# Kernel tuning notes

Measured on AMD Instinct MI355X. Metric: run time of the kernel, lower is better.

Reference implementation:

```python
import jax, jax.numpy as jnp
import numpy as np

B, N = 4, 8192


def setup_inputs() -> dict:
    key = jax.random.key(0)
    k1, k2, k3 = jax.random.split(key, 3)
    pc_pred = jax.random.normal(k1, (B, N, 3), dtype=jnp.float32)
    pc_target = jax.random.normal(k2, (B, N, 3), dtype=jnp.float32)
    fbpp = jax.random.uniform(k3, (B,), dtype=jnp.float32)
    return {"pc_pred": pc_pred, "pc_target": pc_target, "fbpp": fbpp, "lam": 1}


def _chamfer(x, y):
    # x: (B, N, 3), y: (B, M, 3)
    x2 = jnp.sum(x * x, axis=-1)                     # (B, N)
    y2 = jnp.sum(y * y, axis=-1)                     # (B, M)
    xy = jnp.einsum('bnd,bmd->bnm', x, y)            # (B, N, M)
    d2 = jnp.maximum(x2[:, :, None] + y2[:, None, :] - 2.0 * xy, 0.0)
    cham_x = jnp.mean(jnp.min(d2, axis=2), axis=1)   # (B,) pred -> target
    cham_y = jnp.mean(jnp.min(d2, axis=1), axis=1)   # (B,) target -> pred
    return jnp.mean(cham_x + cham_y)                 # scalar (batch mean)


def reference(pc_pred, pc_target, fbpp, lam):
    d = _chamfer(pc_pred, pc_target)
    r = jnp.mean(fbpp)
    return d + lam * r
```

## Files before the change

kernel.cpp:

```cpp
#include <hip/hip_runtime.h>
#include <math.h>


typedef __attribute__((ext_vector_type(8)))  short  short8;
typedef __attribute__((ext_vector_type(16))) float  f32x16;

#define YS      4
#define RPB     256

#define MFMA2(da, db, A, B0, B1) \
    asm("v_mfma_f32_32x32x16_bf16 %0, %2, %3, 0\n\t" \
        "v_mfma_f32_32x32x16_bf16 %1, %2, %4, 0\n\t" \
        "s_nop 7\n\t" \
        "s_nop 7" \
        : "=&v"(da), "=&v"(db) \
        : "v"(A), "v"(B0), "v"(B1))

static __device__ __forceinline__ float min3f(float a, float b, float c) {
    float d;
    asm("v_min3_f32 %0, %1, %2, %3" : "=v"(d) : "v"(a), "v"(b), "v"(c));
    return d;
}

static inline int roundup_h(int v, int a) { return (v + a - 1) / a * a; }

static __device__ __forceinline__ unsigned short f2bf(float f) {
    union { float f; unsigned int u; } v; v.f = f;
    unsigned int r = v.u + 0x7FFFu + ((v.u >> 16) & 1u);
    return (unsigned short)(r >> 16);
}
static __device__ __forceinline__ float bf2f(unsigned short s) {
    union { unsigned int u; float f; } v; v.u = ((unsigned int)s) << 16;
    return v.f;
}
static __device__ __forceinline__ unsigned int pk2(unsigned short lo,
                                                   unsigned short hi) {
    return (unsigned int)lo | ((unsigned int)hi << 16);
}

static __device__ __forceinline__ float allmin32(float v) {
    union { float f; int i; } u, t;
    u.f = v;
    t.i = __builtin_amdgcn_update_dpp(u.i, u.i, 0xB1, 0xF, 0xF, false);
    u.f = fminf(u.f, t.f);
    t.i = __builtin_amdgcn_update_dpp(u.i, u.i, 0x4E, 0xF, 0xF, false);
    u.f = fminf(u.f, t.f);
    t.i = __builtin_amdgcn_update_dpp(u.i, u.i, 0x124, 0xF, 0xF, false);
    u.f = fminf(u.f, t.f);
    t.i = __builtin_amdgcn_update_dpp(u.i, u.i, 0x128, 0xF, 0xF, false);
    u.f = fminf(u.f, t.f);
    t.i = __builtin_amdgcn_ds_swizzle(u.i, 0x401F);
    u.f = fminf(u.f, t.f);
    return u.f;
}

__global__ __launch_bounds__(256) void pack_kernel(
    const float* __restrict__ pred, const float* __restrict__ targ,
    int B, int N, int M, int NpadP, int NpadT,
    unsigned short* __restrict__ aP, unsigned short* __restrict__ bP,
    unsigned short* __restrict__ aT, unsigned short* __restrict__ bT)
{
    const int padmax = (NpadP > NpadT) ? NpadP : NpadT;
    const int gid = blockIdx.x * 256 + threadIdx.x;
    if (gid >= B * padmax) return;
    const int b = gid / padmax, i = gid - b * padmax;

    for (int cloud = 0; cloud < 2; ++cloud) {
        const int cnt  = cloud ? M : N;
        const int npad = cloud ? NpadT : NpadP;
        if (i >= npad) continue;
        const float* src = (cloud ? targ : pred) +
                           ((size_t)b * cnt + min(i, cnt - 1)) * 3;
        unsigned short* A  = (cloud ? aT : aP) + ((size_t)b * npad + i) * 16;
        unsigned short* Bk = (cloud ? bT : bP) + (size_t)b * npad * 16;

        const float xs[3] = {src[0], src[1], src[2]};
        const float n2 = xs[0]*xs[0] + xs[1]*xs[1] + xs[2]*xs[2];
        unsigned short th[3], tl[3], yh[3], yl[3];
        #pragma unroll
        for (int c = 0; c < 3; ++c) {
            const float t = -2.0f * xs[c];
            th[c] = f2bf(t);     tl[c] = f2bf(t - bf2f(th[c]));
            yh[c] = f2bf(xs[c]); yl[c] = f2bf(xs[c] - bf2f(yh[c]));
        }
        const unsigned short n2h = f2bf(n2);
        const unsigned short n2l = f2bf(n2 - bf2f(n2h));
        const unsigned short ONE = 0x3F80;

        uint4 alo, ahi, blo, bhi;
        alo.x = pk2(th[0], th[1]); alo.y = pk2(th[2], tl[0]);
        alo.z = pk2(tl[1], tl[2]); alo.w = pk2(th[0], th[1]);
        ahi.x = pk2(th[2], tl[0]); ahi.y = pk2(tl[1], tl[2]);
        ahi.z = pk2(ONE,  ONE);    ahi.w = pk2(n2h,  n2l);
        blo.x = pk2(yh[0], yh[1]); blo.y = pk2(yh[2], yh[0]);
        blo.z = pk2(yh[1], yh[2]); blo.w = pk2(yl[0], yl[1]);
        bhi.x = pk2(yl[2], yl[0]); bhi.y = pk2(yl[1], yl[2]);
        bhi.z = pk2(n2h,  n2l);    bhi.w = pk2(ONE,  ONE);

        *(uint4*)(A)     = alo;  *(uint4*)(A + 8) = ahi;
        const size_t tb = (size_t)(i >> 5) * 64 + (i & 31);
        *(uint4*)(Bk + tb * 8)        = blo;
        *(uint4*)(Bk + (tb + 32) * 8) = bhi;
    }
}

__global__ __launch_bounds__(256, 4) void mfma_sweep(
    const unsigned short* __restrict__ aP, const unsigned short* __restrict__ bP,
    const unsigned short* __restrict__ aT, const unsigned short* __restrict__ bT,
    int B, int N, int M, int NpadP, int NpadT, int NpadMax,
    float* __restrict__ rowpart)
{
    const int tid  = threadIdx.x;
    const int w    = tid >> 6;
    const int lane = tid & 63;
    const int lc   = lane & 31, h = lane >> 5;

    const int SP = NpadMax / RPB;
    int t = blockIdx.x;
    const int sp  = t % SP;  t /= SP;
    const int js  = t % YS;  t /= YS;
    const int b   = t % B;   t /= B;
    const int dir = t;

    const unsigned short* Xp = (dir == 0) ? aP : aT;
    const unsigned short* Yp = (dir == 0) ? bT : bP;
    const int NpadX = (dir == 0) ? NpadP : NpadT;
    const int NpadY = (dir == 0) ? NpadT : NpadP;
    const int Nx    = (dir == 0) ? N : M;
    if (sp * RPB >= NpadX) return;

    const int TM  = NpadY / 32;
    const int nt0 = TM / YS;
    const int t0  = js * nt0;

    const int row0 = sp * RPB + w * 64;
    const size_t abase = ((size_t)b * NpadX + row0 + lc) * 16 + (size_t)h * 8;
    const short8 a0 = *reinterpret_cast<const short8*>(Xp + abase);
    const short8 a1 = *reinterpret_cast<const short8*>(Xp + abase + 32 * 16);

    f32x16 rm0, rm1;
    #pragma unroll
    for (int r = 0; r < 16; ++r) {
        rm0[r] = __builtin_inff(); rm1[r] = __builtin_inff();
    }

    const unsigned short* yp =
        Yp + (size_t)b * NpadY * 16 + (size_t)t0 * 512 + (size_t)lane * 8;
    short8 c0 = *reinterpret_cast<const short8*>(yp);
    short8 c1 = *reinterpret_cast<const short8*>(yp + 512);

    for (int j = 0; j < nt0; j += 2) {
        const short8 n0 = *reinterpret_cast<const short8*>(yp + 1024);
        const short8 n1 = *reinterpret_cast<const short8*>(yp + 1536);
        yp += 1024;
        __builtin_amdgcn_sched_barrier(0);
        {
            f32x16 da, db;
            MFMA2(da, db, a0, c0, c1);
            #pragma unroll
            for (int r = 0; r < 16; ++r)
                rm0[r] = min3f(da[r], db[r], rm0[r]);
        }
        {
            f32x16 da, db;
            MFMA2(da, db, a1, c0, c1);
            #pragma unroll
            for (int r = 0; r < 16; ++r)
                rm1[r] = min3f(da[r], db[r], rm1[r]);
        }
        c0 = n0; c1 = n1;
    }

    const size_t outb = (((size_t)dir * B + b) * YS + js) * (size_t)NpadMax;
    #pragma unroll
    for (int r = 0; r < 16; ++r) {
        const float v0 = allmin32(rm0[r]);
        const float v1 = allmin32(rm1[r]);
        if (lc == 0) {
            const int rr = (r & 3) + 8 * (r >> 2) + 4 * h;
            const int ra = row0 + rr, rb = row0 + 32 + rr;
            if (ra < Nx) rowpart[outb + ra] = v0;
            if (rb < Nx) rowpart[outb + rb] = v1;
        }
    }
}

__global__ __launch_bounds__(256) void combine_kernel(
    const float* __restrict__ rowpart, int B, int N, int M,
    int NpadP, int NpadT, int NpadMax,
    float invBN, float invBM, float* __restrict__ partial)
{
    const int tid = threadIdx.x;
    const int tot = 2 * B * NpadMax;
    float acc = 0.f;
    for (int idx = blockIdx.x * 256 + tid; idx < tot; idx += gridDim.x * 256) {
        const int row = idx % NpadMax;
        const int rem = idx / NpadMax;
        const int b   = rem % B;
        const int dir = rem / B;
        const int Nx  = (dir == 0) ? N : M;
        if (row >= Nx) continue;
        float m = __builtin_inff();
        #pragma unroll
        for (int js = 0; js < YS; ++js)
            m = fminf(m, rowpart[(((size_t)dir * B + b) * YS + js)
                                 * (size_t)NpadMax + row]);
        acc += fmaxf(m, 0.f) * ((dir == 0) ? invBN : invBM);
    }
    __shared__ float sb[256];
    sb[tid] = acc; __syncthreads();
    for (int off2 = 128; off2 > 0; off2 >>= 1) {
        if (tid < off2) sb[tid] += sb[tid + off2];
        __syncthreads();
    }
    if (tid == 0) partial[blockIdx.x] = sb[0];
}

__global__ void finalize_kernel(const float* __restrict__ partial, int np,
                                const float* __restrict__ fbpp, int Bf,
                                const void* __restrict__ lamp,
                                float* __restrict__ out)
{
    __shared__ float sb[256];
    const int tid = threadIdx.x;
    float acc = 0.f;
    for (int i = tid; i < np; i += 256) acc += partial[i];
    sb[tid] = acc;
    __syncthreads();
    for (int off = 128; off > 0; off >>= 1) {
        if (tid < off) sb[tid] += sb[tid + off];
        __syncthreads();
    }
    if (tid == 0) {
        const int li = *(const int*)lamp;
        const float lam = (li >= -1000000 && li <= 1000000)
                            ? (float)li : *(const float*)lamp;
        float fm = 0.f;
        for (int i = 0; i < Bf; ++i) fm += fbpp[i];
        fm /= (float)Bf;
        out[0] = sb[0] + lam * fm;
    }
}

extern "C" void kernel_launch(void* const* d_in, const int* in_sizes, int n_in,
                              void* d_out, int out_size, void* d_ws, size_t ws_size,
                              hipStream_t stream) {
    const float* pred = (const float*)d_in[0];
    const float* targ = (const float*)d_in[1];
    const float* fbpp = (const float*)d_in[2];
    const void*  lamp = d_in[3];

    const int B = in_sizes[2];
    const int N = in_sizes[0] / (3 * B);
    const int M = in_sizes[1] / (3 * B);
    const int NpadP = roundup_h(N, RPB);
    const int NpadT = roundup_h(M, RPB);
    const int NpadMax = (NpadP > NpadT) ? NpadP : NpadT;

    size_t o = 0;
    auto take = [&](size_t bytes) {
        size_t r = o; o += (bytes + 255) & ~(size_t)255; return r;
    };
    unsigned short* aP = (unsigned short*)((char*)d_ws +
                         take((size_t)B * NpadP * 32 + 8192));
    unsigned short* bP = (unsigned short*)((char*)d_ws +
                         take((size_t)B * NpadP * 32 + 8192));
    unsigned short* aT = (unsigned short*)((char*)d_ws +
                         take((size_t)B * NpadT * 32 + 8192));
    unsigned short* bT = (unsigned short*)((char*)d_ws +
                         take((size_t)B * NpadT * 32 + 8192));
    float* rowpart = (float*)((char*)d_ws +
                     take((size_t)2 * B * YS * NpadMax * sizeof(float)));
    float* partial = (float*)((char*)d_ws + take(256 * sizeof(float)));
    (void)ws_size;

    pack_kernel<<<(B * NpadMax + 255) / 256, 256, 0, stream>>>(
        pred, targ, B, N, M, NpadP, NpadT, aP, bP, aT, bT);

    const int SP = NpadMax / RPB;
    const int blocks = 2 * B * YS * SP;
    mfma_sweep<<<blocks, 256, 0, stream>>>(
        aP, bP, aT, bT, B, N, M, NpadP, NpadT, NpadMax, rowpart);

    combine_kernel<<<256, 256, 0, stream>>>(
        rowpart, B, N, M, NpadP, NpadT, NpadMax,
        1.f / ((float)B * (float)N), 1.f / ((float)B * (float)M), partial);

    finalize_kernel<<<1, 256, 0, stream>>>(partial, 256, fbpp, B, lamp,
                                           (float*)d_out);
}
```

Before: 38.52 us.

## Fuse point packing into the MFMA sweep, staging Y tiles in LDS

Drops the separate pack kernel and its global workspace. Each sweep block now builds its bf16 split A fragments in registers and packs Y tiles into shared memory in chunks of 32 tiles, with block-wide syncs around each chunk. The Y split is doubled to 8 to raise the block count, which shortens each block's loop and doubles the rowpart traffic. This saves one launch and a global round trip, but every block repacks the same Y points and adds LDS reads and barriers inside the hot loop.

Measured after the change: 39.09 us. About the same (+1.5%).

```diff
diff --git a/kernel.cpp b/kernel.cpp
--- a/kernel.cpp
+++ b/kernel.cpp
@@ -5,8 +5,9 @@
 typedef __attribute__((ext_vector_type(8)))  short  short8;
 typedef __attribute__((ext_vector_type(16))) float  f32x16;
 
-#define YS      4
+#define YS      8
 #define RPB     256
+#define LTILES  32
 
 #define MFMA2(da, db, A, B0, B1) \
     asm("v_mfma_f32_32x32x16_bf16 %0, %2, %3, 0\n\t" \
@@ -54,59 +55,25 @@
     return u.f;
 }
 
-__global__ __launch_bounds__(256) void pack_kernel(
+struct PiecesT {
+    unsigned short th[3], tl[3], yh[3], yl[3], n2h, n2l;
+};
+static __device__ __forceinline__ PiecesT pieces(float x, float y, float z) {
+    PiecesT p;
+    const float xs[3] = {x, y, z};
+    const float n2 = x*x + y*y + z*z;
+    #pragma unroll
+    for (int c = 0; c < 3; ++c) {
+        const float t = -2.0f * xs[c];
+        p.th[c] = f2bf(t);      p.tl[c] = f2bf(t - bf2f(p.th[c]));
+        p.yh[c] = f2bf(xs[c]);  p.yl[c] = f2bf(xs[c] - bf2f(p.yh[c]));
+    }
+    p.n2h = f2bf(n2); p.n2l = f2bf(n2 - bf2f(p.n2h));
+    return p;
+}
+
+__global__ __launch_bounds__(256, 4) void fused_sweep(
     const float* __restrict__ pred, const float* __restrict__ targ,
-    int B, int N, int M, int NpadP, int NpadT,
-    unsigned short* __restrict__ aP, unsigned short* __restrict__ bP,
-    unsigned short* __restrict__ aT, unsigned short* __restrict__ bT)
-{
-    const int padmax = (NpadP > NpadT) ? NpadP : NpadT;
-    const int gid = blockIdx.x * 256 + threadIdx.x;
-    if (gid >= B * padmax) return;
-    const int b = gid / padmax, i = gid - b * padmax;
-
-    for (int cloud = 0; cloud < 2; ++cloud) {
-        const int cnt  = cloud ? M : N;
-        const int npad = cloud ? NpadT : NpadP;
-        if (i >= npad) continue;
-        const float* src = (cloud ? targ : pred) +
-                           ((size_t)b * cnt + min(i, cnt - 1)) * 3;
-        unsigned short* A  = (cloud ? aT : aP) + ((size_t)b * npad + i) * 16;
-        unsigned short* Bk = (cloud ? bT : bP) + (size_t)b * npad * 16;
-
-        const float xs[3] = {src[0], src[1], src[2]};
-        const float n2 = xs[0]*xs[0] + xs[1]*xs[1] + xs[2]*xs[2];
-        unsigned short th[3], tl[3], yh[3], yl[3];
-        #pragma unroll
-        for (int c = 0; c < 3; ++c) {
-            const float t = -2.0f * xs[c];
-            th[c] = f2bf(t);     tl[c] = f2bf(t - bf2f(th[c]));
-            yh[c] = f2bf(xs[c]); yl[c] = f2bf(xs[c] - bf2f(yh[c]));
-        }
-        const unsigned short n2h = f2bf(n2);
-        const unsigned short n2l = f2bf(n2 - bf2f(n2h));
-        const unsigned short ONE = 0x3F80;
-
-        uint4 alo, ahi, blo, bhi;
-        alo.x = pk2(th[0], th[1]); alo.y = pk2(th[2], tl[0]);
-        alo.z = pk2(tl[1], tl[2]); alo.w = pk2(th[0], th[1]);
-        ahi.x = pk2(th[2], tl[0]); ahi.y = pk2(tl[1], tl[2]);
-        ahi.z = pk2(ONE,  ONE);    ahi.w = pk2(n2h,  n2l);
-        blo.x = pk2(yh[0], yh[1]); blo.y = pk2(yh[2], yh[0]);
-        blo.z = pk2(yh[1], yh[2]); blo.w = pk2(yl[0], yl[1]);
-        bhi.x = pk2(yl[2], yl[0]); bhi.y = pk2(yl[1], yl[2]);
-        bhi.z = pk2(n2h,  n2l);    bhi.w = pk2(ONE,  ONE);
-
-        *(uint4*)(A)     = alo;  *(uint4*)(A + 8) = ahi;
-        const size_t tb = (size_t)(i >> 5) * 64 + (i & 31);
-        *(uint4*)(Bk + tb * 8)        = blo;
-        *(uint4*)(Bk + (tb + 32) * 8) = bhi;
-    }
-}
-
-__global__ __launch_bounds__(256, 4) void mfma_sweep(
-    const unsigned short* __restrict__ aP, const unsigned short* __restrict__ bP,
-    const unsigned short* __restrict__ aT, const unsigned short* __restrict__ bT,
     int B, int N, int M, int NpadP, int NpadT, int NpadMax,
     float* __restrict__ rowpart)
 {
@@ -122,21 +89,38 @@
     const int b   = t % B;   t /= B;
     const int dir = t;
 
-    const unsigned short* Xp = (dir == 0) ? aP : aT;
-    const unsigned short* Yp = (dir == 0) ? bT : bP;
+    const float* __restrict__ xsrc = (dir == 0) ? pred : targ;
+    const float* __restrict__ ysrc = (dir == 0) ? targ : pred;
+    const int Nx  = (dir == 0) ? N : M;
+    const int My  = (dir == 0) ? M : N;
     const int NpadX = (dir == 0) ? NpadP : NpadT;
     const int NpadY = (dir == 0) ? NpadT : NpadP;
-    const int Nx    = (dir == 0) ? N : M;
     if (sp * RPB >= NpadX) return;
 
     const int TM  = NpadY / 32;
     const int nt0 = TM / YS;
     const int t0  = js * nt0;
 
+    __shared__ unsigned short ypack[LTILES * 32 * 16];
+
+    const unsigned short ONE = 0x3F80;
     const int row0 = sp * RPB + w * 64;
-    const size_t abase = ((size_t)b * NpadX + row0 + lc) * 16 + (size_t)h * 8;
-    const short8 a0 = *reinterpret_cast<const short8*>(Xp + abase);
-    const short8 a1 = *reinterpret_cast<const short8*>(Xp + abase + 32 * 16);
+    short8 a0, a1;
+    #pragma unroll
+    for (int s = 0; s < 2; ++s) {
+        const int row = min(row0 + s * 32 + lc, Nx - 1);
+        const float* sx = xsrc + ((size_t)b * Nx + row) * 3;
+        const PiecesT p = pieces(sx[0], sx[1], sx[2]);
+        short8 v;
+        if (h == 0) {
+            v[0]=p.th[0]; v[1]=p.th[1]; v[2]=p.th[2]; v[3]=p.tl[0];
+            v[4]=p.tl[1]; v[5]=p.tl[2]; v[6]=p.th[0]; v[7]=p.th[1];
+        } else {
+            v[0]=p.th[2]; v[1]=p.tl[0]; v[2]=p.tl[1]; v[3]=p.tl[2];
+            v[4]=ONE;     v[5]=ONE;     v[6]=p.n2h;   v[7]=p.n2l;
+        }
+        if (s == 0) a0 = v; else a1 = v;
+    }
 
     f32x16 rm0, rm1;
     #pragma unroll
@@ -144,31 +128,47 @@
         rm0[r] = __builtin_inff(); rm1[r] = __builtin_inff();
     }
 
-    const unsigned short* yp =
-        Yp + (size_t)b * NpadY * 16 + (size_t)t0 * 512 + (size_t)lane * 8;
-    short8 c0 = *reinterpret_cast<const short8*>(yp);
-    short8 c1 = *reinterpret_cast<const short8*>(yp + 512);
-
-    for (int j = 0; j < nt0; j += 2) {
-        const short8 n0 = *reinterpret_cast<const short8*>(yp + 1024);
-        const short8 n1 = *reinterpret_cast<const short8*>(yp + 1536);
-        yp += 1024;
-        __builtin_amdgcn_sched_barrier(0);
-        {
-            f32x16 da, db;
-            MFMA2(da, db, a0, c0, c1);
-            #pragma unroll
-            for (int r = 0; r < 16; ++r)
-                rm0[r] = min3f(da[r], db[r], rm0[r]);
-        }
-        {
-            f32x16 da, db;
-            MFMA2(da, db, a1, c0, c1);
-            #pragma unroll
-            for (int r = 0; r < 16; ++r)
-                rm1[r] = min3f(da[r], db[r], rm1[r]);
-        }
-        c0 = n0; c1 = n1;
+    for (int f0 = 0; f0 < nt0; f0 += LTILES) {
+        const int fc = min(LTILES, nt0 - f0);
+        __syncthreads();
+        for (int i = tid; i < fc * 32; i += 256) {
+            const int gi  = min((t0 + f0) * 32 + i, My - 1);
+            const float* sy = ysrc + ((size_t)b * My + gi) * 3;
+            const PiecesT p = pieces(sy[0], sy[1], sy[2]);
+            uint4 blo, bhi;
+            blo.x = pk2(p.yh[0], p.yh[1]); blo.y = pk2(p.yh[2], p.yh[0]);
+            blo.z = pk2(p.yh[1], p.yh[2]); blo.w = pk2(p.yl[0], p.yl[1]);
+            bhi.x = pk2(p.yl[2], p.yl[0]); bhi.y = pk2(p.yl[1], p.yl[2]);
+            bhi.z = pk2(p.n2h,  p.n2l);    bhi.w = pk2(ONE,  ONE);
+            const int tile = i >> 5, pos = i & 31;
+            uint4* base = (uint4*)&ypack[(size_t)tile * 512];
+            base[pos]      = blo;
+            base[32 + pos] = bhi;
+        }
+        __syncthreads();
+
+        const unsigned short* lp = ypack + (size_t)lane * 8;
+        #pragma unroll 4
+        for (int j = 0; j < fc; j += 2) {
+            const short8 c0 = *reinterpret_cast<const short8*>(lp + (size_t)j * 512);
+            const short8 c1 = (j + 1 < fc)
+                ? *reinterpret_cast<const short8*>(lp + (size_t)(j + 1) * 512)
+                : c0;
+            {
+                f32x16 da, db;
+                MFMA2(da, db, a0, c0, c1);
+                #pragma unroll
+                for (int r = 0; r < 16; ++r)
+                    rm0[r] = min3f(da[r], db[r], rm0[r]);
+            }
+            {
+                f32x16 da, db;
+                MFMA2(da, db, a1, c0, c1);
+                #pragma unroll
+                for (int r = 0; r < 16; ++r)
+                    rm1[r] = min3f(da[r], db[r], rm1[r]);
+            }
+        }
     }
 
     const size_t outb = (((size_t)dir * B + b) * YS + js) * (size_t)NpadMax;
@@ -187,8 +187,7 @@
 
 __global__ __launch_bounds__(256) void combine_kernel(
     const float* __restrict__ rowpart, int B, int N, int M,
-    int NpadP, int NpadT, int NpadMax,
-    float invBN, float invBM, float* __restrict__ partial)
+    int NpadMax, float invBN, float invBM, float* __restrict__ partial)
 {
     const int tid = threadIdx.x;
     const int tot = 2 * B * NpadMax;
@@ -257,33 +256,17 @@
     const int NpadT = roundup_h(M, RPB);
     const int NpadMax = (NpadP > NpadT) ? NpadP : NpadT;
 
-    size_t o = 0;
-    auto take = [&](size_t bytes) {
-        size_t r = o; o += (bytes + 255) & ~(size_t)255; return r;
-    };
-    unsigned short* aP = (unsigned short*)((char*)d_ws +
-                         take((size_t)B * NpadP * 32 + 8192));
-    unsigned short* bP = (unsigned short*)((char*)d_ws +
-                         take((size_t)B * NpadP * 32 + 8192));
-    unsigned short* aT = (unsigned short*)((char*)d_ws +
-                         take((size_t)B * NpadT * 32 + 8192));
-    unsigned short* bT = (unsigned short*)((char*)d_ws +
-                         take((size_t)B * NpadT * 32 + 8192));
-    float* rowpart = (float*)((char*)d_ws +
-                     take((size_t)2 * B * YS * NpadMax * sizeof(float)));
-    float* partial = (float*)((char*)d_ws + take(256 * sizeof(float)));
+    float* rowpart = (float*)d_ws;
+    float* partial = rowpart + (size_t)2 * B * YS * NpadMax;
     (void)ws_size;
-
-    pack_kernel<<<(B * NpadMax + 255) / 256, 256, 0, stream>>>(
-        pred, targ, B, N, M, NpadP, NpadT, aP, bP, aT, bT);
 
     const int SP = NpadMax / RPB;
     const int blocks = 2 * B * YS * SP;
-    mfma_sweep<<<blocks, 256, 0, stream>>>(
-        aP, bP, aT, bT, B, N, M, NpadP, NpadT, NpadMax, rowpart);
+    fused_sweep<<<blocks, 256, 0, stream>>>(
+        pred, targ, B, N, M, NpadP, NpadT, NpadMax, rowpart);
 
     combine_kernel<<<256, 256, 0, stream>>>(
-        rowpart, B, N, M, NpadP, NpadT, NpadMax,
+        rowpart, B, N, M, NpadMax,
         1.f / ((float)B * (float)N), 1.f / ((float)B * (float)M), partial);
 
     finalize_kernel<<<1, 256, 0, stream>>>(partial, 256, fbpp, B, lamp,
```

## Compute both chamfer directions from one distance sweep via column minima

Applied to the files above, without the earlier changes.

Drops the second (target→pred) MFMA sweep. The single pred×target sweep now also reduces each tile's columns in registers, stages them in a shared-memory buffer, and writes per-row-block column minima to a new colpart array that combine_kernel reduces over SP. This roughly halves the MFMA work and the packing work. In exchange it adds about 32 min3 ops per iteration, a shared buffer that may lower occupancy, and extra colpart memory traffic. The number of column splits YS also goes from 4 to 8 to keep enough blocks in the grid.

Result: slower. 42.78 us (+11.1%).

```diff
diff --git a/kernel.cpp b/kernel.cpp
--- a/kernel.cpp
+++ b/kernel.cpp
@@ -5,7 +5,7 @@
 typedef __attribute__((ext_vector_type(8)))  short  short8;
 typedef __attribute__((ext_vector_type(16))) float  f32x16;
 
-#define YS      4
+#define YS      8
 #define RPB     256
 
 #define MFMA2(da, db, A, B0, B1) \
@@ -57,47 +57,53 @@
 __global__ __launch_bounds__(256) void pack_kernel(
     const float* __restrict__ pred, const float* __restrict__ targ,
     int B, int N, int M, int NpadP, int NpadT,
-    unsigned short* __restrict__ aP, unsigned short* __restrict__ bP,
-    unsigned short* __restrict__ aT, unsigned short* __restrict__ bT)
+    unsigned short* __restrict__ aP, unsigned short* __restrict__ bT)
 {
     const int padmax = (NpadP > NpadT) ? NpadP : NpadT;
     const int gid = blockIdx.x * 256 + threadIdx.x;
     if (gid >= B * padmax) return;
     const int b = gid / padmax, i = gid - b * padmax;
 
-    for (int cloud = 0; cloud < 2; ++cloud) {
-        const int cnt  = cloud ? M : N;
-        const int npad = cloud ? NpadT : NpadP;
-        if (i >= npad) continue;
-        const float* src = (cloud ? targ : pred) +
-                           ((size_t)b * cnt + min(i, cnt - 1)) * 3;
-        unsigned short* A  = (cloud ? aT : aP) + ((size_t)b * npad + i) * 16;
-        unsigned short* Bk = (cloud ? bT : bP) + (size_t)b * npad * 16;
-
+    const unsigned short ONE = 0x3F80;
+
+    if (i < NpadP) {
+        const float* src = pred + ((size_t)b * N + min(i, N - 1)) * 3;
+        unsigned short* A = aP + ((size_t)b * NpadP + i) * 16;
         const float xs[3] = {src[0], src[1], src[2]};
         const float n2 = xs[0]*xs[0] + xs[1]*xs[1] + xs[2]*xs[2];
-        unsigned short th[3], tl[3], yh[3], yl[3];
+        unsigned short th[3], tl[3];
         #pragma unroll
         for (int c = 0; c < 3; ++c) {
             const float t = -2.0f * xs[c];
-            th[c] = f2bf(t);     tl[c] = f2bf(t - bf2f(th[c]));
-            yh[c] = f2bf(xs[c]); yl[c] = f2bf(xs[c] - bf2f(yh[c]));
+            th[c] = f2bf(t); tl[c] = f2bf(t - bf2f(th[c]));
         }
         const unsigned short n2h = f2bf(n2);
         const unsigned short n2l = f2bf(n2 - bf2f(n2h));
-        const unsigned short ONE = 0x3F80;
-
-        uint4 alo, ahi, blo, bhi;
+        uint4 alo, ahi;
         alo.x = pk2(th[0], th[1]); alo.y = pk2(th[2], tl[0]);
         alo.z = pk2(tl[1], tl[2]); alo.w = pk2(th[0], th[1]);
         ahi.x = pk2(th[2], tl[0]); ahi.y = pk2(tl[1], tl[2]);
         ahi.z = pk2(ONE,  ONE);    ahi.w = pk2(n2h,  n2l);
+        *(uint4*)(A) = alo;  *(uint4*)(A + 8) = ahi;
+    }
+
+    if (i < NpadT) {
+        const float* src = targ + ((size_t)b * M + min(i, M - 1)) * 3;
+        unsigned short* Bk = bT + (size_t)b * NpadT * 16;
+        const float xs[3] = {src[0], src[1], src[2]};
+        const float n2 = xs[0]*xs[0] + xs[1]*xs[1] + xs[2]*xs[2];
+        unsigned short yh[3], yl[3];
+        #pragma unroll
+        for (int c = 0; c < 3; ++c) {
+            yh[c] = f2bf(xs[c]); yl[c] = f2bf(xs[c] - bf2f(yh[c]));
+        }
+        const unsigned short n2h = f2bf(n2);
+        const unsigned short n2l = f2bf(n2 - bf2f(n2h));
+        uint4 blo, bhi;
         blo.x = pk2(yh[0], yh[1]); blo.y = pk2(yh[2], yh[0]);
         blo.z = pk2(yh[1], yh[2]); blo.w = pk2(yl[0], yl[1]);
         bhi.x = pk2(yl[2], yl[0]); bhi.y = pk2(yl[1], yl[2]);
         bhi.z = pk2(n2h,  n2l);    bhi.w = pk2(ONE,  ONE);
-
-        *(uint4*)(A)     = alo;  *(uint4*)(A + 8) = ahi;
         const size_t tb = (size_t)(i >> 5) * 64 + (i & 31);
         *(uint4*)(Bk + tb * 8)        = blo;
         *(uint4*)(Bk + (tb + 32) * 8) = bhi;
@@ -105,38 +111,32 @@
 }
 
 __global__ __launch_bounds__(256, 4) void mfma_sweep(
-    const unsigned short* __restrict__ aP, const unsigned short* __restrict__ bP,
-    const unsigned short* __restrict__ aT, const unsigned short* __restrict__ bT,
-    int B, int N, int M, int NpadP, int NpadT, int NpadMax,
-    float* __restrict__ rowpart)
+    const unsigned short* __restrict__ aP, const unsigned short* __restrict__ bT,
+    int B, int N, int M, int NpadP, int NpadT, int NpadMax, int SP,
+    float* __restrict__ rowpart, float* __restrict__ colpart)
 {
     const int tid  = threadIdx.x;
     const int w    = tid >> 6;
     const int lane = tid & 63;
     const int lc   = lane & 31, h = lane >> 5;
 
-    const int SP = NpadMax / RPB;
     int t = blockIdx.x;
     const int sp  = t % SP;  t /= SP;
     const int js  = t % YS;  t /= YS;
-    const int b   = t % B;   t /= B;
-    const int dir = t;
-
-    const unsigned short* Xp = (dir == 0) ? aP : aT;
-    const unsigned short* Yp = (dir == 0) ? bT : bP;
-    const int NpadX = (dir == 0) ? NpadP : NpadT;
-    const int NpadY = (dir == 0) ? NpadT : NpadP;
-    const int Nx    = (dir == 0) ? N : M;
-    if (sp * RPB >= NpadX) return;
-
-    const int TM  = NpadY / 32;
+    const int b   = t;
+
+    if (sp * RPB >= NpadP) return;
+
+    const int TM  = NpadT / 32;
     const int nt0 = TM / YS;
     const int t0  = js * nt0;
 
+    __shared__ float colbuf[8][1024];
+
     const int row0 = sp * RPB + w * 64;
-    const size_t abase = ((size_t)b * NpadX + row0 + lc) * 16 + (size_t)h * 8;
-    const short8 a0 = *reinterpret_cast<const short8*>(Xp + abase);
-    const short8 a1 = *reinterpret_cast<const short8*>(Xp + abase + 32 * 16);
+    const size_t abase = ((size_t)b * NpadP + row0 + lc) * 16 + (size_t)h * 8;
+    const short8 a0 = *reinterpret_cast<const short8*>(aP + abase);
+    const short8 a1 = *reinterpret_cast<const short8*>(aP + abase + 32 * 16);
 
     f32x16 rm0, rm1;
     #pragma unroll
@@ -145,7 +145,7 @@
     }
 
     const unsigned short* yp =
-        Yp + (size_t)b * NpadY * 16 + (size_t)t0 * 512 + (size_t)lane * 8;
+        bT + (size_t)b * NpadT * 16 + (size_t)t0 * 512 + (size_t)lane * 8;
     short8 c0 = *reinterpret_cast<const short8*>(yp);
     short8 c1 = *reinterpret_cast<const short8*>(yp + 512);
 
@@ -154,12 +154,29 @@
         const short8 n1 = *reinterpret_cast<const short8*>(yp + 1536);
         yp += 1024;
         __builtin_amdgcn_sched_barrier(0);
+        float cmA, cmB;
         {
             f32x16 da, db;
             MFMA2(da, db, a0, c0, c1);
             #pragma unroll
             for (int r = 0; r < 16; ++r)
                 rm0[r] = min3f(da[r], db[r], rm0[r]);
+            cmA = min3f(da[0], da[1], da[2]);
+            cmA = min3f(cmA, da[3],  da[4]);
+            cmA = min3f(cmA, da[5],  da[6]);
+            cmA = min3f(cmA, da[7],  da[8]);
+            cmA = min3f(cmA, da[9],  da[10]);
+            cmA = min3f(cmA, da[11], da[12]);
+            cmA = min3f(cmA, da[13], da[14]);
+            cmA = min3f(cmA, da[15], cmA);
+            cmB = min3f(db[0], db[1], db[2]);
+            cmB = min3f(cmB, db[3],  db[4]);
+            cmB = min3f(cmB, db[5],  db[6]);
+            cmB = min3f(cmB, db[7],  db[8]);
+            cmB = min3f(cmB, db[9],  db[10]);
+            cmB = min3f(cmB, db[11], db[12]);
+            cmB = min3f(cmB, db[13], db[14]);
+            cmB = min3f(cmB, db[15], cmB);
         }
         {
             f32x16 da, db;
@@ -167,11 +184,29 @@
             #pragma unroll
             for (int r = 0; r < 16; ++r)
                 rm1[r] = min3f(da[r], db[r], rm1[r]);
-        }
+            cmA = min3f(cmA, da[0],  da[1]);
+            cmA = min3f(cmA, da[2],  da[3]);
+            cmA = min3f(cmA, da[4],  da[5]);
+            cmA = min3f(cmA, da[6],  da[7]);
+            cmA = min3f(cmA, da[8],  da[9]);
+            cmA = min3f(cmA, da[10], da[11]);
+            cmA = min3f(cmA, da[12], da[13]);
+            cmA = min3f(cmA, da[14], da[15]);
+            cmB = min3f(cmB, db[0],  db[1]);
+            cmB = min3f(cmB, db[2],  db[3]);
+            cmB = min3f(cmB, db[4],  db[5]);
+            cmB = min3f(cmB, db[6],  db[7]);
+            cmB = min3f(cmB, db[8],  db[9]);
+            cmB = min3f(cmB, db[10], db[11]);
+            cmB = min3f(cmB, db[12], db[13]);
+            cmB = min3f(cmB, db[14], db[15]);
+        }
+        colbuf[w * 2 + h][j * 32 + lc] = cmA;
+        if (j + 1 < nt0) colbuf[w * 2 + h][(j + 1) * 32 + lc] = cmB;
         c0 = n0; c1 = n1;
     }
 
-    const size_t outb = (((size_t)dir * B + b) * YS + js) * (size_t)NpadMax;
+    const size_t outb = ((size_t)b * YS + js) * (size_t)NpadMax;
     #pragma unroll
     for (int r = 0; r < 16; ++r) {
         const float v0 = allmin32(rm0[r]);
@@ -179,33 +214,51 @@
         if (lc == 0) {
             const int rr = (r & 3) + 8 * (r >> 2) + 4 * h;
             const int ra = row0 + rr, rb = row0 + 32 + rr;
-            if (ra < Nx) rowpart[outb + ra] = v0;
-            if (rb < Nx) rowpart[outb + rb] = v1;
-        }
+            if (ra < N) rowpart[outb + ra] = v0;
+            if (rb < N) rowpart[outb + rb] = v1;
+        }
+    }
+
+    __syncthreads();
+    const int nc = nt0 * 32;
+    const size_t coutb = ((size_t)b * SP + sp) * (size_t)NpadMax;
+    for (int c = tid; c < nc; c += 256) {
+        float m = colbuf[0][c];
+        #pragma unroll
+        for (int s = 1; s < 8; ++s) m = fminf(m, colbuf[s][c]);
+        const int gcol = t0 * 32 + c;
+        if (gcol < M) colpart[coutb + gcol] = m;
     }
 }
 
 __global__ __launch_bounds__(256) void combine_kernel(
-    const float* __restrict__ rowpart, int B, int N, int M,
-    int NpadP, int NpadT, int NpadMax,
+    const float* __restrict__ rowpart, const float* __restrict__ colpart,
+    int B, int N, int M, int NpadMax, int SP,
     float invBN, float invBM, float* __restrict__ partial)
 {
     const int tid = threadIdx.x;
-    const int tot = 2 * B * NpadMax;
+    const int per = B * NpadMax;
+    const int tot = 2 * per;
     float acc = 0.f;
     for (int idx = blockIdx.x * 256 + tid; idx < tot; idx += gridDim.x * 256) {
-        const int row = idx % NpadMax;
-        const int rem = idx / NpadMax;
-        const int b   = rem % B;
-        const int dir = rem / B;
-        const int Nx  = (dir == 0) ? N : M;
-        if (row >= Nx) continue;
-        float m = __builtin_inff();
-        #pragma unroll
-        for (int js = 0; js < YS; ++js)
-            m = fminf(m, rowpart[(((size_t)dir * B + b) * YS + js)
-                                 * (size_t)NpadMax + row]);
-        acc += fmaxf(m, 0.f) * ((dir == 0) ? invBN : invBM);
+        const int half = idx / per;
+        const int rem  = idx - half * per;
+        const int b    = rem / NpadMax;
+        const int p    = rem - b * NpadMax;
+        if (half == 0) {
+            if (p >= N) continue;
+            float m = __builtin_inff();
+            #pragma unroll
+            for (int js = 0; js < YS; ++js)
+                m = fminf(m, rowpart[((size_t)b * YS + js) * NpadMax + p]);
+            acc += fmaxf(m, 0.f) * invBN;
+        } else {
+            if (p >= M) continue;
+            float m = __builtin_inff();
+            for (int s = 0; s < SP; ++s)
+                m = fminf(m, colpart[((size_t)b * SP + s) * NpadMax + p]);
+            acc += fmaxf(m, 0.f) * invBM;
+        }
     }
     __shared__ float sb[256];
     sb[tid] = acc; __syncthreads();
@@ -256,6 +309,7 @@
     const int NpadP = roundup_h(N, RPB);
     const int NpadT = roundup_h(M, RPB);
     const int NpadMax = (NpadP > NpadT) ? NpadP : NpadT;
+    const int SP = NpadP / RPB;
 
     size_t o = 0;
     auto take = [&](size_t bytes) {
@@ -263,27 +317,24 @@
     };
     unsigned short* aP = (unsigned short*)((char*)d_ws +
                          take((size_t)B * NpadP * 32 + 8192));
-    unsigned short* bP = (unsigned short*)((char*)d_ws +
-                         take((size_t)B * NpadP * 32 + 8192));
-    unsigned short* aT = (unsigned short*)((char*)d_ws +
-                         take((size_t)B * NpadT * 32 + 8192));
     unsigned short* bT = (unsigned short*)((char*)d_ws +
                          take((size_t)B * NpadT * 32 + 8192));
     float* rowpart = (float*)((char*)d_ws +
-                     take((size_t)2 * B * YS * NpadMax * sizeof(float)));
+                     take((size_t)B * YS * NpadMax * sizeof(float)));
+    float* colpart = (float*)((char*)d_ws +
+                     take((size_t)B * SP * NpadMax * sizeof(float)));
     float* partial = (float*)((char*)d_ws + take(256 * sizeof(float)));
     (void)ws_size;
 
     pack_kernel<<<(B * NpadMax + 255) / 256, 256, 0, stream>>>(
-        pred, targ, B, N, M, NpadP, NpadT, aP, bP, aT, bT);
-
-    const int SP = NpadMax / RPB;
-    const int blocks = 2 * B * YS * SP;
+        pred, targ, B, N, M, NpadP, NpadT, aP, bT);
+
+    const int blocks = B * YS * SP;
     mfma_sweep<<<blocks, 256, 0, stream>>>(
-        aP, bP, aT, bT, B, N, M, NpadP, NpadT, NpadMax, rowpart);
+        aP, bT, B, N, M, NpadP, NpadT, NpadMax, SP, rowpart, colpart);
 
     combine_kernel<<<256, 256, 0, stream>>>(
-        rowpart, B, N, M, NpadP, NpadT, NpadMax,
+        rowpart, colpart, B, N, M, NpadMax, SP,
         1.f / ((float)B * (float)N), 1.f / ((float)B * (float)M), partial);
 
     finalize_kernel<<<1, 256, 0, stream>>>(partial, 256, fbpp, B, lamp,
```
